# Kernel tuning notes

Measured on AMD Instinct MI355X. Metric: run time of the kernel, lower is better.

The kernel has to match this reference:

```python
import jax, jax.numpy as jnp
import numpy as np

BINS = 10
NUM_CLASSES = 2
BATCH = 8388608


def setup_inputs() -> dict:
    key = jax.random.key(0)
    k1, k2 = jax.random.split(key)
    x = jax.random.normal(k1, (BATCH, NUM_CLASSES), dtype=jnp.float32)
    target = jax.random.randint(k2, (BATCH,), 0, NUM_CLASSES).astype(jnp.int64)
    return {"x": x, "target": target}


def reference(x, target):
    # One-hot targets: y.scatter_(1, target, 1)
    y = jax.nn.one_hot(target, NUM_CLASSES, dtype=x.dtype)  # [B, C]

    # g = |d BCE / d logits| = |sigmoid(x) - y|, detached
    g = jax.lax.stop_gradient(jnp.abs(jax.nn.sigmoid(x) - y))

    # bin_idx = floor(g * (bins - 0.0001)); g in [0,1] -> idx in [0, bins-1]
    bin_idx = jnp.floor(g * (BINS - 0.0001)).astype(jnp.int32)  # [B, C]

    # Single-pass histogram instead of the per-bin Python loop
    bin_count = jnp.zeros((BINS,), dtype=x.dtype).at[bin_idx.reshape(-1)].add(1.0)

    N = x.shape[0] * x.shape[1]
    nonempty = jnp.sum(bin_count > 0).astype(x.dtype)
    gd = jnp.maximum(bin_count * nonempty, 0.0001)
    beta = N / gd  # [bins]

    weight = jax.lax.stop_gradient(beta[bin_idx])  # [B, C], constant wrt x

    # Stable BCE-with-logits, elementwise, then weighted mean (torch semantics)
    bce = jnp.maximum(x, 0.0) - x * y + jnp.log1p(jnp.exp(-jnp.abs(x)))
    return jnp.mean(weight * bce)
```

## Files before the change

kernel.cpp:

```cpp
#include <hip/hip_runtime.h>
#include <math.h>

#define BINS 10

constexpr int   NPAIRS = 4194304;
constexpr float NTOT_F = 16777216.0f;

constexpr int G1  = 1024;
constexpr int BLK = 256;

constexpr size_t WS_SUM = 0;
constexpr size_t WS_CNT = 40960;

__device__ __forceinline__ void proc(float x, bool y1, int tid,
                                     float* __restrict__ lsum,
                                     unsigned* __restrict__ lcnt) {
    float z = y1 ? -x : x;
    float t = __builtin_amdgcn_exp2f(z * 1.4426950408889634f);
    float u = 1.0f + t;
    float g = t * __builtin_amdgcn_rcpf(u);
    int   b = (int)(g * 9.9999f);
    b = b < 9 ? b : 9;
    float l = __builtin_amdgcn_logf(u);
    lsum[b * BLK + tid] += l;
    lcnt[b * BLK + tid] += 1u;
}

__global__ __launch_bounds__(BLK) void ghm_main(const float4* __restrict__ x4,
                                                const int2*   __restrict__ t2,
                                                float*        __restrict__ blk_sum,
                                                unsigned*     __restrict__ blk_cnt) {
    __shared__ float    lsum[BINS * BLK];
    __shared__ unsigned lcnt[BINS * BLK];
    const int tid = threadIdx.x;

#pragma unroll
    for (int b = 0; b < BINS; ++b) {
        lsum[b * BLK + tid] = 0.0f;
        lcnt[b * BLK + tid] = 0u;
    }

    const int stride = gridDim.x * blockDim.x;
    for (int i = blockIdx.x * BLK + tid; i < NPAIRS; i += stride) {
        float4 xv = x4[i];
        int2   tv = t2[i];
        proc(xv.x, tv.x == 0, tid, lsum, lcnt);
        proc(xv.y, tv.x == 1, tid, lsum, lcnt);
        proc(xv.z, tv.y == 0, tid, lsum, lcnt);
        proc(xv.w, tv.y == 1, tid, lsum, lcnt);
    }

    __syncthreads();
    const int wave = tid >> 6;
    const int lane = tid & 63;
    for (int b = wave; b < BINS; b += 4) {
        float    s = lsum[b * BLK + lane]       + lsum[b * BLK + lane + 64]
                   + lsum[b * BLK + lane + 128] + lsum[b * BLK + lane + 192];
        unsigned c = lcnt[b * BLK + lane]       + lcnt[b * BLK + lane + 64]
                   + lcnt[b * BLK + lane + 128] + lcnt[b * BLK + lane + 192];
        for (int off = 32; off > 0; off >>= 1) {
            s += __shfl_down(s, off, 64);
            c += __shfl_down(c, off, 64);
        }
        if (lane == 0) {
            blk_sum[b * G1 + blockIdx.x] = s;
            blk_cnt[b * G1 + blockIdx.x] = c;
        }
    }
}

__global__ __launch_bounds__(640) void ghm_final(const float*    __restrict__ blk_sum,
                                                 const unsigned* __restrict__ blk_cnt,
                                                 float*          __restrict__ out) {
    const int wave = threadIdx.x >> 6;
    const int lane = threadIdx.x & 63;
    double s = 0.0, c = 0.0;
    for (int g = lane; g < G1; g += 64) {
        s += (double)blk_sum[wave * G1 + g];
        c += (double)blk_cnt[wave * G1 + g];
    }
    for (int off = 32; off > 0; off >>= 1) {
        s += __shfl_down(s, off, 64);
        c += __shfl_down(c, off, 64);
    }
    __shared__ double Sb[BINS], Cb[BINS];
    if (lane == 0) { Sb[wave] = s; Cb[wave] = c; }
    __syncthreads();
    if (threadIdx.x == 0) {
        float nonempty = 0.0f;
#pragma unroll
        for (int b = 0; b < BINS; ++b) nonempty += (Cb[b] > 0.0) ? 1.0f : 0.0f;
        double tot = 0.0;
#pragma unroll
        for (int b = 0; b < BINS; ++b) {
            float gd   = fmaxf((float)Cb[b] * nonempty, 0.0001f);
            float beta = NTOT_F / gd;
            tot += (double)beta * Sb[b];
        }
        out[0] = (float)(tot * 0.693147180559945309 / (double)NTOT_F);
    }
}

extern "C" void kernel_launch(void* const* d_in, const int* in_sizes, int n_in,
                              void* d_out, int out_size, void* d_ws, size_t ws_size,
                              hipStream_t stream) {
    const float4* x4 = (const float4*)d_in[0];
    const int2*   t2 = (const int2*)d_in[1];

    float*    blk_sum = (float*)   ((char*)d_ws + WS_SUM);
    unsigned* blk_cnt = (unsigned*)((char*)d_ws + WS_CNT);
    float*    out     = (float*)d_out;

    ghm_main <<<G1, BLK, 0, stream>>>(x4, t2, blk_sum, blk_cnt);
    ghm_final<<<1, 640, 0, stream>>>(blk_sum, blk_cnt, out);
}
```

Before: 122.0 us.

## Interleave LDS sum/count pairs, double grid, fully unroll fixed-trip main loop

Result: slower. 124.6 us (+2.1%).

```diff
diff --git a/kernel.cpp b/kernel.cpp
--- a/kernel.cpp
+++ b/kernel.cpp
@@ -6,15 +6,18 @@
 constexpr int   NPAIRS = 4194304;
 constexpr float NTOT_F = 16777216.0f;
 
-constexpr int G1  = 1024;
-constexpr int BLK = 256;
+constexpr int G1     = 2048;
+constexpr int BLK    = 256;
+constexpr int STRIDE = G1 * BLK;
+constexpr int ITERS  = NPAIRS / STRIDE;
 
 constexpr size_t WS_SUM = 0;
-constexpr size_t WS_CNT = 40960;
+constexpr size_t WS_CNT = 81920;
+
+struct alignas(8) Pair { float s; unsigned c; };
 
 __device__ __forceinline__ void proc(float x, bool y1, int tid,
-                                     float* __restrict__ lsum,
-                                     unsigned* __restrict__ lcnt) {
+                                     Pair* __restrict__ lds) {
     float z = y1 ? -x : x;
     float t = __builtin_amdgcn_exp2f(z * 1.4426950408889634f);
     float u = 1.0f + t;
@@ -22,42 +25,43 @@
     int   b = (int)(g * 9.9999f);
     b = b < 9 ? b : 9;
     float l = __builtin_amdgcn_logf(u);
-    lsum[b * BLK + tid] += l;
-    lcnt[b * BLK + tid] += 1u;
+    Pair  p = lds[b * BLK + tid];
+    p.s += l;
+    p.c += 1u;
+    lds[b * BLK + tid] = p;
 }
 
 __global__ __launch_bounds__(BLK) void ghm_main(const float4* __restrict__ x4,
                                                 const int2*   __restrict__ t2,
                                                 float*        __restrict__ blk_sum,
                                                 unsigned*     __restrict__ blk_cnt) {
-    __shared__ float    lsum[BINS * BLK];
-    __shared__ unsigned lcnt[BINS * BLK];
+    __shared__ Pair lds[BINS * BLK];
     const int tid = threadIdx.x;
 
 #pragma unroll
-    for (int b = 0; b < BINS; ++b) {
-        lsum[b * BLK + tid] = 0.0f;
-        lcnt[b * BLK + tid] = 0u;
-    }
+    for (int b = 0; b < BINS; ++b) lds[b * BLK + tid] = Pair{0.0f, 0u};
 
-    const int stride = gridDim.x * blockDim.x;
-    for (int i = blockIdx.x * BLK + tid; i < NPAIRS; i += stride) {
-        float4 xv = x4[i];
-        int2   tv = t2[i];
-        proc(xv.x, tv.x == 0, tid, lsum, lcnt);
-        proc(xv.y, tv.x == 1, tid, lsum, lcnt);
-        proc(xv.z, tv.y == 0, tid, lsum, lcnt);
-        proc(xv.w, tv.y == 1, tid, lsum, lcnt);
+    const int base = blockIdx.x * BLK + tid;
+#pragma unroll
+    for (int k = 0; k < ITERS; ++k) {
+        float4 xv = x4[base + k * STRIDE];
+        int2   tv = t2[base + k * STRIDE];
+        proc(xv.x, tv.x == 0, tid, lds);
+        proc(xv.y, tv.x == 1, tid, lds);
+        proc(xv.z, tv.y == 0, tid, lds);
+        proc(xv.w, tv.y == 1, tid, lds);
     }
 
     __syncthreads();
     const int wave = tid >> 6;
     const int lane = tid & 63;
     for (int b = wave; b < BINS; b += 4) {
-        float    s = lsum[b * BLK + lane]       + lsum[b * BLK + lane + 64]
-                   + lsum[b * BLK + lane + 128] + lsum[b * BLK + lane + 192];
-        unsigned c = lcnt[b * BLK + lane]       + lcnt[b * BLK + lane + 64]
-                   + lcnt[b * BLK + lane + 128] + lcnt[b * BLK + lane + 192];
+        Pair p0 = lds[b * BLK + lane];
+        Pair p1 = lds[b * BLK + lane + 64];
+        Pair p2 = lds[b * BLK + lane + 128];
+        Pair p3 = lds[b * BLK + lane + 192];
+        float    s = p0.s + p1.s + p2.s + p3.s;
+        unsigned c = p0.c + p1.c + p2.c + p3.c;
         for (int off = 32; off > 0; off >>= 1) {
             s += __shfl_down(s, off, 64);
             c += __shfl_down(c, off, 64);
```
